# Performance work log

Hardware: AMD Instinct MI355X
Metric: run time of the kernel (lower is better)

## Reference

```python
import jax, jax.numpy as jnp
import numpy as np

B, S, D = 4, 2048, 1024
E, H, K = 32, 128, 2


def setup_inputs() -> dict:
    key = jax.random.key(0)
    k1, k2, k3, k4 = jax.random.split(key, 4)
    scale_d = 1.0 / np.sqrt(D)
    scale_h = 1.0 / np.sqrt(H)
    return {
        "x": jax.random.normal(k1, (B, S, D), dtype=jnp.float32),
        "w_sel": jax.random.normal(k2, (E, D), dtype=jnp.float32) * scale_d,      # router Linear weight [E, D]
        "w_keys": jax.random.normal(k3, (E, D, H), dtype=jnp.float32) * scale_d,  # per-expert up-proj
        "w_values": jax.random.normal(k4, (E, H, D), dtype=jnp.float32) * scale_h, # per-expert down-proj
        "k": K,
    }


def reference(x, w_sel, w_keys, w_values, k):
    # Router: sigmoid gating + top-k expert selection per token.
    sel = jax.nn.sigmoid(jnp.einsum('bsd,ed->bse', x, w_sel))      # [B,S,E]
    sel_val, sel_idx = jax.lax.top_k(sel, k)                       # [B,S,k]
    n_exp = w_sel.shape[0]
    # Dense gate matrix: gate[b,s,e] = sum of sel_val over heads routed to e
    # (top_k indices are distinct, so this matches the per-head accumulation).
    gate = jnp.sum(jax.nn.one_hot(sel_idx, n_exp, dtype=x.dtype) * sel_val[..., None], axis=-2)  # [B,S,E]
    # Expert up-projection + ReLU for all experts (dense equivalent of the
    # per-token gathered keys[expert_idx](token); unselected experts are
    # zeroed by the gate so the math is identical).
    scores = jax.nn.relu(jnp.einsum('bsd,edh->bseh', x, w_keys))   # [B,S,E,H]
    weighted = scores * gate[..., None]                            # [B,S,E,H]
    out = jnp.einsum('bseh,ehd->bsd', weighted, w_values)          # [B,S,D]
    return out
```

## Files before the change

kernel.cpp:

```cpp
#include <hip/hip_runtime.h>
#include <cstdint>
#include <cstddef>

#define NTOK 8192
#define DIM  1024
#define NEXP 32
#define NH   128
#define TT   64
#define FTILES 16
#define BK   128
#define RT   32
#define LCAP 1024

typedef __attribute__((ext_vector_type(8))) short short8;
typedef __attribute__((ext_vector_type(4))) float float4_;

static __device__ __forceinline__ unsigned short f2bf(float f) {
  unsigned u = __float_as_uint(f);
  return (unsigned short)((u + 0x7fffu + ((u >> 16) & 1u)) >> 16);
}
static __device__ __forceinline__ float bf2f(unsigned short h) {
  return __uint_as_float(((unsigned)h) << 16);
}
static __device__ __forceinline__ void gload_lds16(const unsigned short* g,
                                                   unsigned short* l) {
  __builtin_amdgcn_global_load_lds(
      (const __attribute__((address_space(1))) unsigned int*)(const void*)g,
      (__attribute__((address_space(3))) unsigned int*)(void*)l, 16, 0, 0);
}

__global__ __launch_bounds__(256) void prep_kernel(
    const float* __restrict__ w_keys, const float* __restrict__ w_values,
    const float* __restrict__ x,
    unsigned short* __restrict__ wk_t, unsigned short* __restrict__ wv_t,
    unsigned short* __restrict__ xbf, int* __restrict__ counts)
{
  __shared__ float tile[32][33];
  const int bid = blockIdx.x;
  const int tid = threadIdx.x;
  if (bid == 0 && tid < NEXP) counts[tid] = 0;

  if (bid < 8192) {
    const float* src; unsigned short* dst; int R, C, lb;
    if (bid < 4096) { src = w_keys;   dst = wk_t; R = DIM; C = NH;  lb = bid; }
    else            { src = w_values; dst = wv_t; R = NH;  C = DIM; lb = bid - 4096; }
    const int e  = lb >> 7;
    const int t  = lb & 127;
    const int tpc = C >> 5;
    const int r0 = (t / tpc) * 32;
    const int c0 = (t % tpc) * 32;
    const float* s = src + (size_t)e * R * C;
    unsigned short* d = dst + (size_t)e * R * C;

    const int i = tid >> 3;
    const int j = (tid & 7) * 4;
    float4 v = *(const float4*)(s + (size_t)(r0 + i) * C + c0 + j);
    tile[i][j] = v.x; tile[i][j + 1] = v.y; tile[i][j + 2] = v.z; tile[i][j + 3] = v.w;
    __syncthreads();
    unsigned lo = (unsigned)f2bf(tile[j + 0][i]) | ((unsigned)f2bf(tile[j + 1][i]) << 16);
    unsigned hi = (unsigned)f2bf(tile[j + 2][i]) | ((unsigned)f2bf(tile[j + 3][i]) << 16);
    uint2 u; u.x = lo; u.y = hi;
    *(uint2*)(d + (size_t)(c0 + i) * R + r0 + j) = u;
  } else {
    const int lb = bid - 8192;
    size_t i = ((size_t)lb * 256 + tid) * 8;
    float4 a = *(const float4*)(x + i);
    float4 b = *(const float4*)(x + i + 4);
    uint4 u;
    u.x = (unsigned)f2bf(a.x) | ((unsigned)f2bf(a.y) << 16);
    u.y = (unsigned)f2bf(a.z) | ((unsigned)f2bf(a.w) << 16);
    u.z = (unsigned)f2bf(b.x) | ((unsigned)f2bf(b.y) << 16);
    u.w = (unsigned)f2bf(b.z) | ((unsigned)f2bf(b.w) << 16);
    *(uint4*)(xbf + i) = u;
  }
}

__global__ __launch_bounds__(256) void router_kernel(
    const float* __restrict__ x, const float* __restrict__ w_sel,
    int* __restrict__ counts, unsigned* __restrict__ list)
{
  __shared__ __align__(16) float xs_t[64][36];
  __shared__ float ws[NEXP][65];
  __shared__ float S[RT][33];

  const int tid  = threadIdx.x;
  const int tok0 = blockIdx.x * RT;
  const int tr   = tid >> 3;
  const int d8   = (tid & 7) * 8;
  const int tg4  = (tid & 7) * 4;

  float acc[4] = {0.f, 0.f, 0.f, 0.f};

  for (int dc = 0; dc < DIM; dc += 64) {
    const float* xp = x + (size_t)(tok0 + tr) * DIM + dc + d8;
    float4 a0 = *(const float4*)(xp);
    float4 a1 = *(const float4*)(xp + 4);
    xs_t[d8 + 0][tr] = a0.x; xs_t[d8 + 1][tr] = a0.y;
    xs_t[d8 + 2][tr] = a0.z; xs_t[d8 + 3][tr] = a0.w;
    xs_t[d8 + 4][tr] = a1.x; xs_t[d8 + 5][tr] = a1.y;
    xs_t[d8 + 6][tr] = a1.z; xs_t[d8 + 7][tr] = a1.w;
    const float* wp = w_sel + (size_t)tr * DIM + dc + d8;
    float4 b0 = *(const float4*)(wp);
    float4 b1 = *(const float4*)(wp + 4);
    ws[tr][d8 + 0] = b0.x; ws[tr][d8 + 1] = b0.y;
    ws[tr][d8 + 2] = b0.z; ws[tr][d8 + 3] = b0.w;
    ws[tr][d8 + 4] = b1.x; ws[tr][d8 + 5] = b1.y;
    ws[tr][d8 + 6] = b1.z; ws[tr][d8 + 7] = b1.w;
    __syncthreads();

    #pragma unroll 8
    for (int d = 0; d < 64; ++d) {
      float w = ws[tr][d];
      float4 xv = *(const float4*)&xs_t[d][tg4];
      acc[0] += xv.x * w; acc[1] += xv.y * w;
      acc[2] += xv.z * w; acc[3] += xv.w * w;
    }
    __syncthreads();
  }

  #pragma unroll
  for (int j = 0; j < 4; ++j)
    S[tg4 + j][tr] = acc[j];
  __syncthreads();

  if (tid < RT) {
    const int t = tid;
    float m1 = -1e30f, m2 = -1e30f;
    int i1 = 0, i2 = 0;
    for (int ee = 0; ee < NEXP; ++ee) {
      float v = S[t][ee];
      if (v > m1)      { m2 = m1; i2 = i1; m1 = v; i1 = ee; }
      else if (v > m2) { m2 = v; i2 = ee; }
    }
    const int token = tok0 + t;
    float g1 = 1.f / (1.f + __expf(-m1));
    float g2 = 1.f / (1.f + __expf(-m2));
    unsigned e1 = ((unsigned)f2bf(g1) << 16) | ((unsigned)token << 1);
    unsigned e2 = ((unsigned)f2bf(g2) << 16) | ((unsigned)token << 1) | 1u;
    int p1 = atomicAdd(&counts[i1], 1);
    if (p1 < LCAP) list[i1 * LCAP + p1] = e1;
    int p2 = atomicAdd(&counts[i2], 1);
    if (p2 < LCAP) list[i2 * LCAP + p2] = e2;
  }
}

__global__ __launch_bounds__(256, 2) void ffn_kernel(
    const unsigned short* __restrict__ xbf,
    const unsigned short* __restrict__ wk_t,
    const unsigned short* __restrict__ wv_t,
    float* __restrict__ out,
    unsigned short* __restrict__ cont,
    const int* __restrict__ counts, const unsigned* __restrict__ list,
    int use_cont)
{
  const int bid = blockIdx.x;
  const int e   = bid & 31;
  const int cnt = min(counts[e], LCAP);

  __shared__ unsigned short xsf[2][16 * 512];
  __shared__ unsigned short ss[TT][NH + 8];
  __shared__ int   toks[TT];
  __shared__ float gates[TT];

  const int tid  = threadIdx.x;
  const int wave = tid >> 6;
  const int lane = tid & 63;
  const int quad = lane >> 4;
  const int l16  = lane & 15;

  const unsigned short* wkb = wk_t + (size_t)e * NH * DIM;
  const unsigned short* wvb = wv_t + (size_t)e * DIM * NH;

  for (int t0 = (bid >> 5) * TT; t0 < cnt; t0 += FTILES * TT) {
    const int n_tok = min(TT, cnt - t0);

    if (tid < TT) {
      int valid = tid < n_tok;
      unsigned en = valid ? list[e * LCAP + t0 + tid] : 0u;
      toks[tid]  = valid ? (int)(en & 0xffffu) : -1;
      gates[tid] = valid ? bf2f((unsigned short)(en >> 16)) : 0.f;
    }
    __syncthreads();

    int slot = toks[wave * 16 + l16];
    int gtok = (slot < 0) ? 0 : (slot >> 1);
    const unsigned short* gsrc = xbf + (size_t)gtok * DIM + quad * 8;

    #pragma unroll
    for (int kk = 0; kk < 4; ++kk)
      gload_lds16(gsrc + kk * 32, &xsf[0][(wave * 4 + kk) * 512]);
    __syncthreads();

    float4_ acc[4][2];
    #pragma unroll
    for (int mt = 0; mt < 4; ++mt)
      #pragma unroll
      for (int nt = 0; nt < 2; ++nt) acc[mt][nt] = (float4_){0.f, 0.f, 0.f, 0.f};

    for (int ci = 0; ci < 8; ++ci) {
      const int dc = ci * BK;
      if (ci < 7) {
        const int nb = (ci + 1) & 1;
        #pragma unroll
        for (int kk = 0; kk < 4; ++kk)
          gload_lds16(gsrc + dc + BK + kk * 32, &xsf[nb][(wave * 4 + kk) * 512]);
      }
      short8 b[4][2];
      #pragma unroll
      for (int kk = 0; kk < 4; ++kk)
        #pragma unroll
        for (int nt = 0; nt < 2; ++nt)
          b[kk][nt] = *(const short8*)(wkb +
              (size_t)(wave * 32 + nt * 16 + l16) * DIM + dc + kk * 32 + quad * 8);

      const unsigned short* xb = &xsf[ci & 1][0];
      #pragma unroll
      for (int kk = 0; kk < 4; ++kk) {
        #pragma unroll
        for (int mt = 0; mt < 4; ++mt) {
          short8 a = *(const short8*)(xb + (mt * 4 + kk) * 512 + lane * 8);
          #pragma unroll
          for (int nt = 0; nt < 2; ++nt)
            acc[mt][nt] = __builtin_amdgcn_mfma_f32_16x16x32_bf16(a, b[kk][nt], acc[mt][nt], 0, 0, 0);
        }
      }
      __syncthreads();
    }

    #pragma unroll
    for (int mt = 0; mt < 4; ++mt)
      #pragma unroll
      for (int nt = 0; nt < 2; ++nt)
        #pragma unroll
        for (int r = 0; r < 4; ++r) {
          int row = mt * 16 + quad * 4 + r;
          float v = fmaxf(acc[mt][nt][r], 0.f) * gates[row];
          ss[row][wave * 32 + nt * 16 + l16] = f2bf(v);
        }
    __syncthreads();

    #pragma unroll 1
    for (int nc = 0; nc < 4; ++nc) {
      const int colbase = wave * 256 + nc * 64;
      float4_ o[4][4];
      #pragma unroll
      for (int mt = 0; mt < 4; ++mt)
        #pragma unroll
        for (int nt = 0; nt < 4; ++nt) o[mt][nt] = (float4_){0.f, 0.f, 0.f, 0.f};

      short8 b2[4][4];
      #pragma unroll
      for (int kk = 0; kk < 4; ++kk)
        #pragma unroll
        for (int nt = 0; nt < 4; ++nt)
          b2[kk][nt] = *(const short8*)(wvb +
              (size_t)(colbase + nt * 16 + l16) * NH + kk * 32 + quad * 8);

      #pragma unroll
      for (int kk = 0; kk < 4; ++kk) {
        short8 a[4];
        #pragma unroll
        for (int mt = 0; mt < 4; ++mt)
          a[mt] = *(const short8*)&ss[mt * 16 + l16][kk * 32 + quad * 8];
        #pragma unroll
        for (int mt = 0; mt < 4; ++mt)
          #pragma unroll
          for (int nt = 0; nt < 4; ++nt)
            o[mt][nt] = __builtin_amdgcn_mfma_f32_16x16x32_bf16(a[mt], b2[kk][nt], o[mt][nt], 0, 0, 0);
      }

      if (use_cont) {
        #pragma unroll
        for (int mt = 0; mt < 4; ++mt)
          #pragma unroll
          for (int r = 0; r < 4; ++r) {
            int row = mt * 16 + quad * 4 + r;
            if (row < n_tok) {
              int sl = toks[row];
              size_t base = ((size_t)((sl & 1) * NTOK + (sl >> 1))) * DIM + colbase;
              #pragma unroll
              for (int nt = 0; nt < 4; ++nt)
                cont[base + nt * 16 + l16] = f2bf(o[mt][nt][r]);
            }
          }
      } else {
        #pragma unroll
        for (int mt = 0; mt < 4; ++mt)
          #pragma unroll
          for (int r = 0; r < 4; ++r) {
            int row = mt * 16 + quad * 4 + r;
            if (row < n_tok) {
              size_t base = (size_t)(toks[row] >> 1) * DIM + colbase;
              #pragma unroll
              for (int nt = 0; nt < 4; ++nt)
                unsafeAtomicAdd(&out[base + nt * 16 + l16], o[mt][nt][r]);
            }
          }
      }
    }
    __syncthreads();
  }
}

__global__ __launch_bounds__(256) void combine_kernel(
    const unsigned short* __restrict__ cont, float* __restrict__ out)
{
  size_t i = ((size_t)blockIdx.x * 256 + threadIdx.x) * 8;
  uint4 a = *(const uint4*)(cont + i);
  uint4 b = *(const uint4*)(cont + (size_t)NTOK * DIM + i);
  float4 r0, r1;
  r0.x = bf2f((unsigned short)(a.x & 0xffff)) + bf2f((unsigned short)(b.x & 0xffff));
  r0.y = bf2f((unsigned short)(a.x >> 16))    + bf2f((unsigned short)(b.x >> 16));
  r0.z = bf2f((unsigned short)(a.y & 0xffff)) + bf2f((unsigned short)(b.y & 0xffff));
  r0.w = bf2f((unsigned short)(a.y >> 16))    + bf2f((unsigned short)(b.y >> 16));
  r1.x = bf2f((unsigned short)(a.z & 0xffff)) + bf2f((unsigned short)(b.z & 0xffff));
  r1.y = bf2f((unsigned short)(a.z >> 16))    + bf2f((unsigned short)(b.z >> 16));
  r1.z = bf2f((unsigned short)(a.w & 0xffff)) + bf2f((unsigned short)(b.w & 0xffff));
  r1.w = bf2f((unsigned short)(a.w >> 16))    + bf2f((unsigned short)(b.w >> 16));
  *(float4*)(out + i) = r0;
  *(float4*)(out + i + 4) = r1;
}

extern "C" void kernel_launch(void* const* d_in, const int* in_sizes, int n_in,
                              void* d_out, int out_size, void* d_ws, size_t ws_size,
                              hipStream_t stream) {
  (void)in_sizes; (void)n_in;
  const float* x        = (const float*)d_in[0];
  const float* w_sel    = (const float*)d_in[1];
  const float* w_keys   = (const float*)d_in[2];
  const float* w_values = (const float*)d_in[3];
  float* out = (float*)d_out;

  char* ws = (char*)d_ws;
  size_t off = 0;
  int*            counts = (int*)(ws + off);            off += 4096;
  unsigned*       list   = (unsigned*)(ws + off);       off += (size_t)NEXP * LCAP * 4;
  unsigned short* wk_t   = (unsigned short*)(ws + off); off += (size_t)NEXP * NH * DIM * 2;
  unsigned short* wv_t   = (unsigned short*)(ws + off); off += (size_t)NEXP * NH * DIM * 2;
  unsigned short* xbf    = (unsigned short*)(ws + off); off += (size_t)NTOK * DIM * 2;
  unsigned short* cont   = (unsigned short*)(ws + off);
  size_t need_full = off + (size_t)2 * NTOK * DIM * 2;
  const int use_cont = (ws_size >= need_full) ? 1 : 0;

  prep_kernel<<<12288, 256, 0, stream>>>(w_keys, w_values, x, wk_t, wv_t, xbf, counts);

  router_kernel<<<NTOK / RT, 256, 0, stream>>>(x, w_sel, counts, list);

  if (!use_cont)
    hipMemsetAsync(out, 0, (size_t)out_size * sizeof(float), stream);

  ffn_kernel<<<NEXP * FTILES, 256, 0, stream>>>(xbf, wk_t, wv_t, out, cont,
                                                counts, list, use_cont);

  if (use_cont)
    combine_kernel<<<NTOK * DIM / (256 * 8), 256, 0, stream>>>(cont, out);
}
```

Measured before the change: 251.3 us.

## Fuse prep and router kernels, shrink FFN tiles, stage coalesced output stores

Merges the weight transpose/convert kernel and the router kernel into one launch, with the router blocks also writing the bf16 copy of x, so x is read only once. The FFN kernel moves from a persistent loop over 64-token tiles to one 32-token tile per block over 32 slots per expert, with higher occupancy launch bounds and early exit for empty slots. Output tiles are staged through shared memory so the contribution buffer is written with 16-byte coalesced stores instead of scattered 2-byte stores. Smaller tiles reuse the weights less per load and add barriers, and there is an extra memset launch for counts.

```diff
diff --git a/kernel.cpp b/kernel.cpp
--- a/kernel.cpp
+++ b/kernel.cpp
@@ -6,8 +6,8 @@
 #define DIM  1024
 #define NEXP 32
 #define NH   128
-#define TT   64
-#define FTILES 16
+#define TT   32
+#define NSLOT 32
 #define BK   128
 #define RT   32
 #define LCAP 1024
@@ -29,23 +29,22 @@
       (__attribute__((address_space(3))) unsigned int*)(void*)l, 16, 0, 0);
 }
 
-__global__ __launch_bounds__(256) void prep_kernel(
+__global__ __launch_bounds__(256) void prep_router_kernel(
+    const float* __restrict__ x, const float* __restrict__ w_sel,
     const float* __restrict__ w_keys, const float* __restrict__ w_values,
-    const float* __restrict__ x,
-    unsigned short* __restrict__ wk_t, unsigned short* __restrict__ wv_t,
-    unsigned short* __restrict__ xbf, int* __restrict__ counts)
+    unsigned short* __restrict__ xbf, unsigned short* __restrict__ wk_t,
+    unsigned short* __restrict__ wv_t,
+    int* __restrict__ counts, unsigned* __restrict__ list)
 {
-  __shared__ float tile[32][33];
   const int bid = blockIdx.x;
   const int tid = threadIdx.x;
-  if (bid == 0 && tid < NEXP) counts[tid] = 0;
-
-  if (bid < 8192) {
-    const float* src; unsigned short* dst; int R, C, lb;
-    if (bid < 4096) { src = w_keys;   dst = wk_t; R = DIM; C = NH;  lb = bid; }
-    else            { src = w_values; dst = wv_t; R = NH;  C = DIM; lb = bid - 4096; }
-    const int e  = lb >> 7;
-    const int t  = lb & 127;
+
+  if (bid >= 256) {
+    __shared__ float tile[32][33];
+    const int lb = bid - 256;
+    const float* src; unsigned short* dst; int R, C, e, t;
+    if (lb < 4096) { src = w_keys;   dst = wk_t; R = DIM; C = NH;  e = lb >> 7;          t = lb & 127; }
+    else           { src = w_values; dst = wv_t; R = NH;  C = DIM; e = (lb - 4096) >> 7; t = (lb - 4096) & 127; }
     const int tpc = C >> 5;
     const int r0 = (t / tpc) * 32;
     const int c0 = (t % tpc) * 32;
@@ -61,30 +60,14 @@
     unsigned hi = (unsigned)f2bf(tile[j + 2][i]) | ((unsigned)f2bf(tile[j + 3][i]) << 16);
     uint2 u; u.x = lo; u.y = hi;
     *(uint2*)(d + (size_t)(c0 + i) * R + r0 + j) = u;
-  } else {
-    const int lb = bid - 8192;
-    size_t i = ((size_t)lb * 256 + tid) * 8;
-    float4 a = *(const float4*)(x + i);
-    float4 b = *(const float4*)(x + i + 4);
-    uint4 u;
-    u.x = (unsigned)f2bf(a.x) | ((unsigned)f2bf(a.y) << 16);
-    u.y = (unsigned)f2bf(a.z) | ((unsigned)f2bf(a.w) << 16);
-    u.z = (unsigned)f2bf(b.x) | ((unsigned)f2bf(b.y) << 16);
-    u.w = (unsigned)f2bf(b.z) | ((unsigned)f2bf(b.w) << 16);
-    *(uint4*)(xbf + i) = u;
-  }
-}
-
-__global__ __launch_bounds__(256) void router_kernel(
-    const float* __restrict__ x, const float* __restrict__ w_sel,
-    int* __restrict__ counts, unsigned* __restrict__ list)
-{
+    return;
+  }
+
   __shared__ __align__(16) float xs_t[64][36];
   __shared__ float ws[NEXP][65];
   __shared__ float S[RT][33];
 
-  const int tid  = threadIdx.x;
-  const int tok0 = blockIdx.x * RT;
+  const int tok0 = bid * RT;
   const int tr   = tid >> 3;
   const int d8   = (tid & 7) * 8;
   const int tg4  = (tid & 7) * 4;
@@ -99,6 +82,13 @@
     xs_t[d8 + 2][tr] = a0.z; xs_t[d8 + 3][tr] = a0.w;
     xs_t[d8 + 4][tr] = a1.x; xs_t[d8 + 5][tr] = a1.y;
     xs_t[d8 + 6][tr] = a1.z; xs_t[d8 + 7][tr] = a1.w;
+    uint4 u;
+    u.x = (unsigned)f2bf(a0.x) | ((unsigned)f2bf(a0.y) << 16);
+    u.y = (unsigned)f2bf(a0.z) | ((unsigned)f2bf(a0.w) << 16);
+    u.z = (unsigned)f2bf(a1.x) | ((unsigned)f2bf(a1.y) << 16);
+    u.w = (unsigned)f2bf(a1.z) | ((unsigned)f2bf(a1.w) << 16);
+    *(uint4*)(xbf + (size_t)(tok0 + tr) * DIM + dc + d8) = u;
+
     const float* wp = w_sel + (size_t)tr * DIM + dc + d8;
     float4 b0 = *(const float4*)(wp);
     float4 b1 = *(const float4*)(wp + 4);
@@ -109,9 +99,9 @@
     __syncthreads();
 
     #pragma unroll 8
-    for (int d = 0; d < 64; ++d) {
-      float w = ws[tr][d];
-      float4 xv = *(const float4*)&xs_t[d][tg4];
+    for (int dd = 0; dd < 64; ++dd) {
+      float w = ws[tr][dd];
+      float4 xv = *(const float4*)&xs_t[dd][tg4];
       acc[0] += xv.x * w; acc[1] += xv.y * w;
       acc[2] += xv.z * w; acc[3] += xv.w * w;
     }
@@ -144,7 +134,7 @@
   }
 }
 
-__global__ __launch_bounds__(256, 2) void ffn_kernel(
+__global__ __launch_bounds__(256, 4) void ffn_kernel(
     const unsigned short* __restrict__ xbf,
     const unsigned short* __restrict__ wk_t,
     const unsigned short* __restrict__ wv_t,
@@ -156,11 +146,15 @@
   const int bid = blockIdx.x;
   const int e   = bid & 31;
   const int cnt = min(counts[e], LCAP);
-
-  __shared__ unsigned short xsf[2][16 * 512];
+  const int t0  = (bid >> 5) * TT;
+  if (t0 >= cnt) return;
+
+  __shared__ __align__(16) unsigned short uni[8448];
   __shared__ unsigned short ss[TT][NH + 8];
   __shared__ int   toks[TT];
   __shared__ float gates[TT];
+  unsigned short (*xsf)[4096] = (unsigned short (*)[4096])uni;
+  unsigned short (*st)[264]   = (unsigned short (*)[264])uni;
 
   const int tid  = threadIdx.x;
   const int wave = tid >> 6;
@@ -170,30 +164,31 @@
 
   const unsigned short* wkb = wk_t + (size_t)e * NH * DIM;
   const unsigned short* wvb = wv_t + (size_t)e * DIM * NH;
-
-  for (int t0 = (bid >> 5) * TT; t0 < cnt; t0 += FTILES * TT) {
-    const int n_tok = min(TT, cnt - t0);
-
-    if (tid < TT) {
-      int valid = tid < n_tok;
-      unsigned en = valid ? list[e * LCAP + t0 + tid] : 0u;
-      toks[tid]  = valid ? (int)(en & 0xffffu) : -1;
-      gates[tid] = valid ? bf2f((unsigned short)(en >> 16)) : 0.f;
-    }
+  const int n_tok = min(TT, cnt - t0);
+
+  if (tid < TT) {
+    int valid = tid < n_tok;
+    unsigned en = valid ? list[e * LCAP + t0 + tid] : 0u;
+    toks[tid]  = valid ? (int)(en & 0xffffu) : -1;
+    gates[tid] = valid ? bf2f((unsigned short)(en >> 16)) : 0.f;
+  }
+  __syncthreads();
+
+  const int smt  = wave >> 1;
+  const int skk0 = (wave & 1) * 2;
+  {
+    int sl   = toks[smt * 16 + l16];
+    int gtok = (sl < 0) ? 0 : (sl >> 1);
+    const unsigned short* gsrc = xbf + (size_t)gtok * DIM + quad * 8;
+
+    #pragma unroll
+    for (int i2 = 0; i2 < 2; ++i2)
+      gload_lds16(gsrc + (skk0 + i2) * 32, &xsf[0][(smt * 4 + skk0 + i2) * 512]);
     __syncthreads();
 
-    int slot = toks[wave * 16 + l16];
-    int gtok = (slot < 0) ? 0 : (slot >> 1);
-    const unsigned short* gsrc = xbf + (size_t)gtok * DIM + quad * 8;
-
-    #pragma unroll
-    for (int kk = 0; kk < 4; ++kk)
-      gload_lds16(gsrc + kk * 32, &xsf[0][(wave * 4 + kk) * 512]);
-    __syncthreads();
-
-    float4_ acc[4][2];
-    #pragma unroll
-    for (int mt = 0; mt < 4; ++mt)
+    float4_ acc[2][2];
+    #pragma unroll
+    for (int mt = 0; mt < 2; ++mt)
       #pragma unroll
       for (int nt = 0; nt < 2; ++nt) acc[mt][nt] = (float4_){0.f, 0.f, 0.f, 0.f};
 
@@ -202,8 +197,9 @@
       if (ci < 7) {
         const int nb = (ci + 1) & 1;
         #pragma unroll
-        for (int kk = 0; kk < 4; ++kk)
-          gload_lds16(gsrc + dc + BK + kk * 32, &xsf[nb][(wave * 4 + kk) * 512]);
+        for (int i2 = 0; i2 < 2; ++i2)
+          gload_lds16(gsrc + dc + BK + (skk0 + i2) * 32,
+                      &xsf[nb][(smt * 4 + skk0 + i2) * 512]);
       }
       short8 b[4][2];
       #pragma unroll
@@ -217,7 +213,7 @@
       #pragma unroll
       for (int kk = 0; kk < 4; ++kk) {
         #pragma unroll
-        for (int mt = 0; mt < 4; ++mt) {
+        for (int mt = 0; mt < 2; ++mt) {
           short8 a = *(const short8*)(xb + (mt * 4 + kk) * 512 + lane * 8);
           #pragma unroll
           for (int nt = 0; nt < 2; ++nt)
@@ -228,7 +224,7 @@
     }
 
     #pragma unroll
-    for (int mt = 0; mt < 4; ++mt)
+    for (int mt = 0; mt < 2; ++mt)
       #pragma unroll
       for (int nt = 0; nt < 2; ++nt)
         #pragma unroll
@@ -237,68 +233,69 @@
           float v = fmaxf(acc[mt][nt][r], 0.f) * gates[row];
           ss[row][wave * 32 + nt * 16 + l16] = f2bf(v);
         }
-    __syncthreads();
-
-    #pragma unroll 1
-    for (int nc = 0; nc < 4; ++nc) {
-      const int colbase = wave * 256 + nc * 64;
-      float4_ o[4][4];
-      #pragma unroll
-      for (int mt = 0; mt < 4; ++mt)
-        #pragma unroll
-        for (int nt = 0; nt < 4; ++nt) o[mt][nt] = (float4_){0.f, 0.f, 0.f, 0.f};
-
-      short8 b2[4][4];
-      #pragma unroll
-      for (int kk = 0; kk < 4; ++kk)
+  }
+  __syncthreads();
+
+  #pragma unroll 1
+  for (int nc = 0; nc < 4; ++nc) {
+    const int colbase = wave * 256 + nc * 64;
+    float4_ o[2][4];
+    #pragma unroll
+    for (int mt = 0; mt < 2; ++mt)
+      #pragma unroll
+      for (int nt = 0; nt < 4; ++nt) o[mt][nt] = (float4_){0.f, 0.f, 0.f, 0.f};
+
+    #pragma unroll
+    for (int kk = 0; kk < 4; ++kk) {
+      short8 bk[4];
+      #pragma unroll
+      for (int nt = 0; nt < 4; ++nt)
+        bk[nt] = *(const short8*)(wvb +
+            (size_t)(colbase + nt * 16 + l16) * NH + kk * 32 + quad * 8);
+      short8 a0 = *(const short8*)&ss[l16][kk * 32 + quad * 8];
+      short8 a1 = *(const short8*)&ss[16 + l16][kk * 32 + quad * 8];
+      #pragma unroll
+      for (int nt = 0; nt < 4; ++nt) {
+        o[0][nt] = __builtin_amdgcn_mfma_f32_16x16x32_bf16(a0, bk[nt], o[0][nt], 0, 0, 0);
+        o[1][nt] = __builtin_amdgcn_mfma_f32_16x16x32_bf16(a1, bk[nt], o[1][nt], 0, 0, 0);
+      }
+    }
+
+    if (use_cont) {
+      #pragma unroll
+      for (int mt = 0; mt < 2; ++mt)
         #pragma unroll
         for (int nt = 0; nt < 4; ++nt)
-          b2[kk][nt] = *(const short8*)(wvb +
-              (size_t)(colbase + nt * 16 + l16) * NH + kk * 32 + quad * 8);
-
-      #pragma unroll
-      for (int kk = 0; kk < 4; ++kk) {
-        short8 a[4];
-        #pragma unroll
-        for (int mt = 0; mt < 4; ++mt)
-          a[mt] = *(const short8*)&ss[mt * 16 + l16][kk * 32 + quad * 8];
-        #pragma unroll
-        for (int mt = 0; mt < 4; ++mt)
           #pragma unroll
-          for (int nt = 0; nt < 4; ++nt)
-            o[mt][nt] = __builtin_amdgcn_mfma_f32_16x16x32_bf16(a[mt], b2[kk][nt], o[mt][nt], 0, 0, 0);
+          for (int r = 0; r < 4; ++r)
+            st[mt * 16 + quad * 4 + r][wave * 64 + nt * 16 + l16] = f2bf(o[mt][nt][r]);
+      __syncthreads();
+      #pragma unroll
+      for (int q = 0; q < 4; ++q) {
+        int idx = q * 256 + tid;
+        int row = idx >> 5, seg = idx & 31;
+        if (row < n_tok) {
+          int sl2 = toks[row];
+          size_t base = ((size_t)((sl2 & 1) * NTOK + (sl2 >> 1))) * DIM
+                        + (seg >> 3) * 256 + nc * 64 + (seg & 7) * 8;
+          *(short8*)&cont[base] = *(const short8*)&st[row][seg * 8];
+        }
       }
-
-      if (use_cont) {
-        #pragma unroll
-        for (int mt = 0; mt < 4; ++mt)
-          #pragma unroll
-          for (int r = 0; r < 4; ++r) {
-            int row = mt * 16 + quad * 4 + r;
-            if (row < n_tok) {
-              int sl = toks[row];
-              size_t base = ((size_t)((sl & 1) * NTOK + (sl >> 1))) * DIM + colbase;
-              #pragma unroll
-              for (int nt = 0; nt < 4; ++nt)
-                cont[base + nt * 16 + l16] = f2bf(o[mt][nt][r]);
-            }
+      __syncthreads();
+    } else {
+      #pragma unroll
+      for (int mt = 0; mt < 2; ++mt)
+        #pragma unroll
+        for (int r = 0; r < 4; ++r) {
+          int row = mt * 16 + quad * 4 + r;
+          if (row < n_tok) {
+            size_t base = (size_t)(toks[row] >> 1) * DIM + colbase;
+            #pragma unroll
+            for (int nt = 0; nt < 4; ++nt)
+              unsafeAtomicAdd(&out[base + nt * 16 + l16], o[mt][nt][r]);
           }
-      } else {
-        #pragma unroll
-        for (int mt = 0; mt < 4; ++mt)
-          #pragma unroll
-          for (int r = 0; r < 4; ++r) {
-            int row = mt * 16 + quad * 4 + r;
-            if (row < n_tok) {
-              size_t base = (size_t)(toks[row] >> 1) * DIM + colbase;
-              #pragma unroll
-              for (int nt = 0; nt < 4; ++nt)
-                unsafeAtomicAdd(&out[base + nt * 16 + l16], o[mt][nt][r]);
-            }
-          }
-      }
-    }
-    __syncthreads();
+        }
+    }
   }
 }
 
@@ -342,15 +339,16 @@
   size_t need_full = off + (size_t)2 * NTOK * DIM * 2;
   const int use_cont = (ws_size >= need_full) ? 1 : 0;
 
-  prep_kernel<<<12288, 256, 0, stream>>>(w_keys, w_values, x, wk_t, wv_t, xbf, counts);
-
-  router_kernel<<<NTOK / RT, 256, 0, stream>>>(x, w_sel, counts, list);
+  hipMemsetAsync(counts, 0, NEXP * sizeof(int), stream);
+
+  prep_router_kernel<<<256 + 8192, 256, 0, stream>>>(x, w_sel, w_keys, w_values,
+                                                     xbf, wk_t, wv_t, counts, list);
 
   if (!use_cont)
     hipMemsetAsync(out, 0, (size_t)out_size * sizeof(float), stream);
 
-  ffn_kernel<<<NEXP * FTILES, 256, 0, stream>>>(xbf, wk_t, wv_t, out, cont,
-                                                counts, list, use_cont);
+  ffn_kernel<<<NEXP * NSLOT, 256, 0, stream>>>(xbf, wk_t, wv_t, out, cont,
+                                               counts, list, use_cont);
 
   if (use_cont)
     combine_kernel<<<NTOK * DIM / (256 * 8), 256, 0, stream>>>(cont, out);
```

Result: faster. 225.6 us (-10.2%).
